# Kernel optimization log

Measured on AMD Instinct MI355X. Metric: run time of the kernel, lower is better.

## Reference

```python
import jax, jax.numpy as jnp
import numpy as np

D_MODEL = 768
N_HEADS = 12
D_K = D_MODEL // N_HEADS
WINDOW = 256
NEG_INF = -1e30


def setup_inputs() -> dict:
    key = jax.random.key(0)
    ks = jax.random.split(key, 9)
    s = 0.02
    x = jax.random.normal(ks[0], (2, 2048, D_MODEL), dtype=jnp.float32)
    Wq = jax.random.normal(ks[1], (D_MODEL, D_MODEL), dtype=jnp.float32) * s
    bq = jnp.zeros((D_MODEL,), dtype=jnp.float32)
    Wk = jax.random.normal(ks[2], (D_MODEL, D_MODEL), dtype=jnp.float32) * s
    bk = jnp.zeros((D_MODEL,), dtype=jnp.float32)
    Wv = jax.random.normal(ks[3], (D_MODEL, D_MODEL), dtype=jnp.float32) * s
    bv = jnp.zeros((D_MODEL,), dtype=jnp.float32)
    Wo = jax.random.normal(ks[4], (D_MODEL, D_MODEL), dtype=jnp.float32) * s
    bo = jnp.zeros((D_MODEL,), dtype=jnp.float32)
    return {"x": x, "Wq": Wq, "bq": bq, "Wk": Wk, "bk": bk,
            "Wv": Wv, "bv": bv, "Wo": Wo, "bo": bo}


def _window_mask(seq_len: int) -> jnp.ndarray:
    # Faithful to _apply_sliding_window_attention: scores are reshaped into
    # (nw, ws, nw, ws) windows and a causal tril is applied broadcast over BOTH
    # window indices => position (q, k) allowed iff (q % ws) >= (k % ws).
    # (seq_len here is a multiple of WINDOW, so pad/slice is a no-op.)
    if seq_len <= WINDOW:
        q = jnp.arange(seq_len)
        return q[:, None] >= jnp.arange(seq_len)[None, :]
    qmod = jnp.arange(seq_len) % WINDOW
    return qmod[:, None] >= qmod[None, :]


def reference(x, Wq, bq, Wk, bk, Wv, bv, Wo, bo):
    B, S, _ = x.shape
    # torch nn.Linear: y = x @ W.T + b
    q = (x @ Wq.T + bq).reshape(B, S, N_HEADS, D_K).transpose(0, 2, 1, 3)
    k = (x @ Wk.T + bk).reshape(B, S, N_HEADS, D_K).transpose(0, 2, 1, 3)
    v = (x @ Wv.T + bv).reshape(B, S, N_HEADS, D_K).transpose(0, 2, 1, 3)
    scores = jnp.einsum('bhqd,bhkd->bhqk', q, k) / jnp.sqrt(jnp.float32(D_K))
    mask = _window_mask(S)  # [S, S] bool
    scores = jnp.where(mask[None, None, :, :], scores, NEG_INF)
    probs = jax.nn.softmax(scores, axis=-1)  # dropout p=0 (eval)
    out = jnp.einsum('bhqk,bhkd->bhqd', probs, v)
    out = out.transpose(0, 2, 1, 3).reshape(B, S, D_MODEL)
    return out @ Wo.T + bo
```

## Files before the change

kernel.cpp:

```cpp
#include <hip/hip_runtime.h>

typedef unsigned short u16;
typedef unsigned int u32;
typedef unsigned long long u64;
typedef __attribute__((ext_vector_type(8))) short bfrag;
typedef __attribute__((ext_vector_type(4))) float f32x4;
typedef __attribute__((ext_vector_type(16))) float f32x16;
typedef __attribute__((ext_vector_type(4))) u32 u32x4;

#define QSCALE 0.18033688f

__device__ __forceinline__ u16 f2bf(float f) {
    unsigned u = __float_as_uint(f);
    u += 0x7FFFu + ((u >> 16) & 1u);
    return (u16)(u >> 16);
}

__device__ __forceinline__ u32 cvt_pk_bf16(float lo, float hi) {
    u32 r;
    asm("v_cvt_pk_bf16_f32 %0, %1, %2" : "=v"(r) : "v"(lo), "v"(hi));
    return r;
}

__device__ __forceinline__ void glds16(const void* g, void* l) {
    __builtin_amdgcn_global_load_lds((__attribute__((address_space(1))) void*)g,
                                     (__attribute__((address_space(3))) void*)l,
                                     16, 0, 0);
}

__device__ __forceinline__ f32x16 mfma32(bfrag a, bfrag b, f32x16 c) {
    return __builtin_amdgcn_mfma_f32_32x32x16_bf16(a, b, c, 0, 0, 0);
}

#define WAIT_VM4()  asm volatile("s_waitcnt vmcnt(4)" ::: "memory")
#define WAIT_VM0()  asm volatile("s_waitcnt vmcnt(0)" ::: "memory")
#define BAR()       __builtin_amdgcn_s_barrier()
#define SCHED_FENCE() __builtin_amdgcn_sched_barrier(0)

__global__ __launch_bounds__(256) void convert_all(
    const float* __restrict__ x, const float* __restrict__ wq,
    const float* __restrict__ wk, const float* __restrict__ wv,
    const float* __restrict__ wo,
    u16* __restrict__ xb, u16* __restrict__ wqb, u16* __restrict__ wkb,
    u16* __restrict__ wvb, u16* __restrict__ wob) {
    const int XV = (2 * 2048 * 768) / 4;
    const int WV = (768 * 768) / 4;
    int i = blockIdx.x * 256 + threadIdx.x;
    if (i >= XV + 4 * WV) return;
    const float4* src; u16* dst; int off;
    if (i < XV) { src = (const float4*)x; dst = xb; off = i; }
    else {
        int j = i - XV; int z = j / WV; off = j - z * WV;
        src = (const float4*)(z == 0 ? wq : z == 1 ? wk : z == 2 ? wv : wo);
        dst = (z == 0 ? wqb : z == 1 ? wkb : z == 2 ? wvb : wob);
    }
    float4 v = src[off];
    u64 pk = (u64)f2bf(v.x)
        | ((u64)f2bf(v.y) << 16)
        | ((u64)f2bf(v.z) << 32)
        | ((u64)f2bf(v.w) << 48);
    *(u64*)(dst + off * 4) = pk;
}

__device__ __forceinline__ void gemm_core(
    const u16* __restrict__ A, const u16* __restrict__ Bw, int m0,
    u16* a_lds, u16* b_lds, f32x4 acc[4][4]) {
    const int t = threadIdx.x;
    const int w = t >> 6, lane = t & 63, ln = lane & 15, lh = lane >> 4;
    const int wr = w >> 1, wc = w & 1;

    const int row0 = t >> 2;
    const int u0 = (t & 3) ^ ((row0 >> 1) & 3);
    const int row1 = row0 + 64;
    const int u1 = (t & 3) ^ ((row1 >> 1) & 3);
    const u16* ga0 = A + (m0 + row0) * 768 + u0 * 8;
    const u16* ga1 = A + (m0 + row1) * 768 + u1 * 8;
    const u16* gb0 = Bw + row0 * 768 + u0 * 8;
    const u16* gb1 = Bw + row1 * 768 + u1 * 8;
    u16* la = a_lds + w * 512;
    u16* lb = b_lds + w * 512;

    auto STAGE = [&](int k0, int bi) {
        glds16(ga0 + k0, la + bi * 4096);
        glds16(ga1 + k0, la + bi * 4096 + 2048);
        glds16(gb0 + k0, lb + bi * 4096);
        glds16(gb1 + k0, lb + bi * 4096 + 2048);
    };

    STAGE(0, 0);
    int cur = 0;
    for (int k0 = 0; k0 < 768; k0 += 32) {
        if (k0 + 32 < 768) {
            STAGE(k0 + 32, cur ^ 1);
            WAIT_VM4();
        } else {
            WAIT_VM0();
        }
        BAR();
        SCHED_FENCE();
        const u16* ab = a_lds + cur * 4096;
        const u16* bb = b_lds + cur * 4096;
        bfrag aF[4], bF[4];
#pragma unroll
        for (int i = 0; i < 4; i++) {
            int ra = wr * 64 + i * 16 + ln;
            aF[i] = *(const bfrag*)(ab + ra * 32 + ((lh ^ ((ra >> 1) & 3)) * 8));
            int rb = wc * 64 + i * 16 + ln;
            bF[i] = *(const bfrag*)(bb + rb * 32 + ((lh ^ ((rb >> 1) & 3)) * 8));
        }
#pragma unroll
        for (int i = 0; i < 4; i++)
#pragma unroll
            for (int j = 0; j < 4; j++)
                acc[i][j] = __builtin_amdgcn_mfma_f32_16x16x32_bf16(
                    aF[i], bF[j], acc[i][j], 0, 0, 0);
        SCHED_FENCE();
        BAR();
        cur ^= 1;
    }
}

__global__ __launch_bounds__(256) void gemm_qkv(
    const u16* __restrict__ xb,
    const u16* __restrict__ wqb, const u16* __restrict__ wkb, const u16* __restrict__ wvb,
    const float* __restrict__ bq, const float* __restrict__ bk, const float* __restrict__ bv,
    u16* __restrict__ q_ws, u16* __restrict__ k_ws, u16* __restrict__ vt_ws) {
    __shared__ __align__(16) u16 smem[16384];
    u16* a_lds = smem;
    u16* b_lds = smem + 8192;
    const int m0 = blockIdx.x * 128;
    const int z = blockIdx.y / 6, nb = blockIdx.y % 6;
    const u16* Bw = (z == 0 ? wqb : z == 1 ? wkb : wvb) + nb * 128 * 768;
    const float* bias = (z == 0 ? bq : z == 1 ? bk : bv);

    f32x4 acc[4][4] = {};
    gemm_core(xb, Bw, m0, a_lds, b_lds, acc);

    const int t = threadIdx.x, w = t >> 6, lane = t & 63, ln = lane & 15, lh = lane >> 4;
    const int wr = w >> 1, wc = w & 1;
    if (z == 2) {
        __syncthreads();
        char* T = (char*)smem;
#pragma unroll
        for (int j = 0; j < 4; j++) {
            int nt = wc * 64 + j * 16 + ln;
            float bb = bias[nb * 128 + nt];
#pragma unroll
            for (int i = 0; i < 4; i++) {
                int m0t = wr * 64 + i * 16 + lh * 4;
                u64 pk = (u64)f2bf(acc[i][j][0] + bb)
                    | ((u64)f2bf(acc[i][j][1] + bb) << 16)
                    | ((u64)f2bf(acc[i][j][2] + bb) << 32)
                    | ((u64)f2bf(acc[i][j][3] + bb) << 48);
                int off = nt * 256 + ((m0t * 2) ^ ((nt & 15) << 4));
                *(u64*)(T + off) = pk;
            }
        }
        __syncthreads();
        const int b = m0 >> 11, s0 = m0 & 2047;
#pragma unroll
        for (int c = 0; c < 8; c++) {
            int g = c * 256 + t;
            int nt = g >> 4, mc = (g & 15) * 8;
            int off = nt * 256 + ((mc * 2) ^ ((nt & 15) << 4));
            u32x4 v = *(const u32x4*)(T + off);
            int nl = nb * 128 + nt;
            int h = nl >> 6, d = nl & 63;
            *(u32x4*)(vt_ws + ((size_t)((b * 12 + h) * 64 + d)) * 2048 + s0 + mc) = v;
        }
    } else {
        u16* dst = (z == 0 ? q_ws : k_ws);
        const float sc = (z == 0) ? QSCALE : 1.0f;
#pragma unroll
        for (int j = 0; j < 4; j++) {
            int nl = nb * 128 + wc * 64 + j * 16 + ln;
            int h = nl >> 6, d = nl & 63;
            float bb = bias[nl];
#pragma unroll
            for (int i = 0; i < 4; i++)
#pragma unroll
                for (int r = 0; r < 4; r++) {
                    int m = m0 + wr * 64 + i * 16 + lh * 4 + r;
                    int b = m >> 11, s = m & 2047;
                    dst[((size_t)((b * 12 + h) * 2048 + s)) * 64 + d] = f2bf((acc[i][j][r] + bb) * sc);
                }
        }
    }
}

__global__ __launch_bounds__(256) void gemm_out(
    const u16* __restrict__ ob, const u16* __restrict__ wob,
    const float* __restrict__ bo, float* __restrict__ out) {
    __shared__ __align__(16) u16 a_lds[2 * 128 * 32];
    __shared__ __align__(16) u16 b_lds[2 * 128 * 32];
    const int m0 = blockIdx.x * 128, n0 = blockIdx.y * 128;
    f32x4 acc[4][4] = {};
    gemm_core(ob, wob + n0 * 768, m0, a_lds, b_lds, acc);
    const int t = threadIdx.x, w = t >> 6, lane = t & 63, ln = lane & 15, lh = lane >> 4;
    const int wr = w >> 1, wc = w & 1;
#pragma unroll
    for (int j = 0; j < 4; j++) {
        int n = n0 + wc * 64 + j * 16 + ln;
        float bb = bo[n];
#pragma unroll
        for (int i = 0; i < 4; i++)
#pragma unroll
            for (int r = 0; r < 4; r++) {
                int m = m0 + wr * 64 + i * 16 + lh * 4 + r;
                out[m * 768 + n] = acc[i][j][r] + bb;
            }
    }
}

__global__ __launch_bounds__(256) void attn7(
    const u16* __restrict__ q_ws, const u16* __restrict__ k_ws,
    const u16* __restrict__ vt_ws,
    u16* __restrict__ po_ws, float* __restrict__ l_ws) {
    __shared__ __align__(16) u16 k_lds[2][64 * 64];
    __shared__ __align__(16) u16 v_lds[2][64 * 64];

    const int t = threadIdx.x, w = t >> 6, l = t & 63, lq = l & 31, H = l >> 5;
    int id = blockIdx.x;
    int bh8 = id & 7, idq = id >> 3;
    int bhq = idq % 3, pg = idq / 3;
    int t7, rem;
    if (pg < 16)      { t7 = 7 - (pg >> 3); rem = pg & 7; }
    else if (pg < 28) { int u = pg - 16; t7 = 5 - u / 6; rem = u % 6; }
    else if (pg < 36) { int u = pg - 28; t7 = 3 - (u >> 2); rem = u & 3; }
    else              { int u = pg - 36; t7 = 1 - (u >> 1); rem = u & 1; }
    const int np = (t7 + 2) >> 1;
    const int quad = rem / np, piece = rem - quad * np;
    const int bh = bhq * 8 + bh8;
    const int ti = quad * 4 + w;
    const int tile = t7 + 8 * ti;
    const int qw0 = tile * 32;

    const u16* Qb = q_ws + (size_t)bh * 2048 * 64;
    const u16* Kb = k_ws + (size_t)bh * 2048 * 64;
    const u16* Vt = vt_ws + (size_t)bh * 64 * 2048;

    const int lqp = (lq & 19) | ((lq & 4) << 1) | ((lq & 8) >> 1);
    const int ksw = lqp & 7;
    const int vsw = lq & 7;

    bfrag qF[4];
#pragma unroll
    for (int kd = 0; kd < 4; kd++)
        qF[kd] = *(const bfrag*)(Qb + (size_t)(qw0 + lq) * 64 + kd * 16 + H * 8);

    const f32x16 Z = {};
    f32x16 O0 = Z, O1 = Z;
    float lsum = 0.f;

    const int skey = t >> 3;
    const int su = (t & 7) ^ (skey & 7);

    auto STAGE = [&](int k0, int bi) {
        glds16(Kb + (size_t)(k0 + skey) * 64 + su * 8,        k_lds[bi] + w * 512);
        glds16(Kb + (size_t)(k0 + skey + 32) * 64 + su * 8,   k_lds[bi] + 2048 + w * 512);
        glds16(Vt + (size_t)skey * 2048 + k0 + su * 8,        v_lds[bi] + w * 512);
        glds16(Vt + (size_t)(skey + 32) * 2048 + k0 + su * 8, v_lds[bi] + 2048 + w * 512);
    };

    int gp0 = piece * 8;
    int win = gp0 / np, pb = gp0 - win * np;
    STAGE(win * 256 + pb * 64, 0);

    for (int j = 0; j < 8; ++j) {
        int winn = win, pbn = pb + 1;
        if (pbn == np) { pbn = 0; winn = win + 1; }
        if (j < 7) {
            STAGE(winn * 256 + pbn * 64, (j + 1) & 1);
            WAIT_VM4();
        } else {
            WAIT_VM0();
        }
        BAR();
        SCHED_FENCE();

        const int cb = 2 * pb;
        const bool c1 = (cb + 1) <= t7, d0 = (cb == t7), d1 = (cb + 1 == t7);
        const u16* kl = k_lds[j & 1];
        const u16* vl = v_lds[j & 1];

        f32x16 s0, s1;
        {
            bfrag kf = *(const bfrag*)(kl + lqp * 64 + ((H) ^ ksw) * 8);
            s0 = mfma32(kf, qF[0], Z);
#pragma unroll
            for (int kd = 1; kd < 4; kd++) {
                bfrag k2 = *(const bfrag*)(kl + lqp * 64 + ((kd * 2 + H) ^ ksw) * 8);
                s0 = mfma32(k2, qF[kd], s0);
            }
        }
        if (c1) {
            bfrag kf = *(const bfrag*)(kl + (32 + lqp) * 64 + ((H) ^ ksw) * 8);
            s1 = mfma32(kf, qF[0], Z);
#pragma unroll
            for (int kd = 1; kd < 4; kd++) {
                bfrag k2 = *(const bfrag*)(kl + (32 + lqp) * 64 + ((kd * 2 + H) ^ ksw) * 8);
                s1 = mfma32(k2, qF[kd], s1);
            }
        }

        float ps = 0.f;
        u32 pkA[8], pkB[8];
        if (d0) {
#pragma unroll
            for (int r2 = 0; r2 < 16; r2++) {
                int ka = (r2 & 3) + 4 * ((r2 >> 2) & 1) + 16 * (r2 >> 3) + 8 * H;
                if (ka > lq) s0[r2] = -1e30f;
            }
        }
#pragma unroll
        for (int i = 0; i < 8; i++) {
            float a = exp2f(s0[2 * i]), b2 = exp2f(s0[2 * i + 1]);
            ps += a + b2; pkA[i] = cvt_pk_bf16(a, b2);
        }
        if (c1) {
            if (d1) {
#pragma unroll
                for (int r2 = 0; r2 < 16; r2++) {
                    int ka = (r2 & 3) + 4 * ((r2 >> 2) & 1) + 16 * (r2 >> 3) + 8 * H;
                    if (ka > lq) s1[r2] = -1e30f;
                }
            }
#pragma unroll
            for (int i = 0; i < 8; i++) {
                float a = exp2f(s1[2 * i]), b2 = exp2f(s1[2 * i + 1]);
                ps += a + b2; pkB[i] = cvt_pk_bf16(a, b2);
            }
        }
        lsum += ps;

        {
            u32x4 a0 = {pkA[0], pkA[1], pkA[2], pkA[3]};
            u32x4 a1 = {pkA[4], pkA[5], pkA[6], pkA[7]};
            bfrag A0 = __builtin_bit_cast(bfrag, a0);
            bfrag A1 = __builtin_bit_cast(bfrag, a1);
            bfrag v00 = *(const bfrag*)(vl + lq * 64 + ((H) ^ vsw) * 8);
            bfrag v01 = *(const bfrag*)(vl + (32 + lq) * 64 + ((H) ^ vsw) * 8);
            bfrag v10 = *(const bfrag*)(vl + lq * 64 + ((2 + H) ^ vsw) * 8);
            bfrag v11 = *(const bfrag*)(vl + (32 + lq) * 64 + ((2 + H) ^ vsw) * 8);
            O0 = mfma32(A0, v00, O0);
            O1 = mfma32(A0, v01, O1);
            O0 = mfma32(A1, v10, O0);
            O1 = mfma32(A1, v11, O1);
        }
        if (c1) {
            u32x4 a0 = {pkB[0], pkB[1], pkB[2], pkB[3]};
            u32x4 a1 = {pkB[4], pkB[5], pkB[6], pkB[7]};
            bfrag A0 = __builtin_bit_cast(bfrag, a0);
            bfrag A1 = __builtin_bit_cast(bfrag, a1);
            bfrag v00 = *(const bfrag*)(vl + lq * 64 + ((4 + H) ^ vsw) * 8);
            bfrag v01 = *(const bfrag*)(vl + (32 + lq) * 64 + ((4 + H) ^ vsw) * 8);
            bfrag v10 = *(const bfrag*)(vl + lq * 64 + ((6 + H) ^ vsw) * 8);
            bfrag v11 = *(const bfrag*)(vl + (32 + lq) * 64 + ((6 + H) ^ vsw) * 8);
            O0 = mfma32(A0, v00, O0);
            O1 = mfma32(A0, v01, O1);
            O0 = mfma32(A1, v10, O0);
            O1 = mfma32(A1, v11, O1);
        }
        SCHED_FENCE();
        BAR();
        win = winn; pb = pbn;
    }

    const int cum8[8] = {0, 8, 16, 32, 48, 72, 96, 128};
    size_t pidx = (size_t)bh * 160 + cum8[t7] + ti * np + piece;
    u16* po = po_ws + pidx * 2048;
#pragma unroll
    for (int r2 = 0; r2 < 16; r2++) {
        int row = (r2 & 3) + 8 * (r2 >> 2) + 4 * H;
        po[row * 64 + lq] = f2bf(O0[r2]);
        po[row * 64 + 32 + lq] = f2bf(O1[r2]);
    }
    float lsT = lsum + __shfl_xor(lsum, 32);
    if (l < 32) l_ws[pidx * 32 + lq] = lsT;
}

__global__ __launch_bounds__(256) void combine_o(
    const u16* __restrict__ po_ws, const float* __restrict__ l_ws,
    u16* __restrict__ o_ws) {
    int id = blockIdx.x;
    int bh8 = id & 7, idq = id >> 3;
    int bhq = idq % 3, r = idq / 3;
    int bh = bhq * 8 + bh8;
    int t7 = r >> 3, ti = r & 7;
    int tile = t7 + 8 * ti;
    int np = (t7 + 2) >> 1;
    const int cum8[8] = {0, 8, 16, 32, 48, 72, 96, 128};
    size_t base = (size_t)bh * 160 + cum8[t7] + ti * np;
    int t = threadIdx.x;
    int q = t >> 3, d8 = (t & 7) * 8;
    float acc[8] = {0.f, 0.f, 0.f, 0.f, 0.f, 0.f, 0.f, 0.f};
    float lt = 0.f;
    for (int i = 0; i < np; i++) {
        lt += l_ws[(base + i) * 32 + q];
        bfrag v = *(const bfrag*)(po_ws + (base + i) * 2048 + q * 64 + d8);
#pragma unroll
        for (int e = 0; e < 8; e++)
            acc[e] += __uint_as_float(((u32)(u16)v[e]) << 16);
    }
    float inv = 1.f / lt;
    u32x4 pkv;
#pragma unroll
    for (int e = 0; e < 4; e++)
        pkv[e] = cvt_pk_bf16(acc[2 * e] * inv, acc[2 * e + 1] * inv);
    int b = bh / 12, h = bh % 12;
    size_t dst = ((size_t)(b * 2048 + tile * 32 + q)) * 768 + h * 64 + d8;
    *(u32x4*)(o_ws + dst) = pkv;
}

extern "C" void kernel_launch(void* const* d_in, const int* in_sizes, int n_in,
                              void* d_out, int out_size, void* d_ws, size_t ws_size,
                              hipStream_t stream) {
    const float* x  = (const float*)d_in[0];
    const float* Wq = (const float*)d_in[1];
    const float* bq = (const float*)d_in[2];
    const float* Wk = (const float*)d_in[3];
    const float* bk = (const float*)d_in[4];
    const float* Wv = (const float*)d_in[5];
    const float* bv = (const float*)d_in[6];
    const float* Wo = (const float*)d_in[7];
    const float* bo = (const float*)d_in[8];
    float* out = (float*)d_out;

    char* p = (char*)d_ws;
    u16*   q_ws  = (u16*)(p + 0);
    u16*   k_ws  = (u16*)(p + 6291456);
    u16*   vt_ws = (u16*)(p + 12582912);
    u16*   po_ws = (u16*)(p + 18874368);
    u16*   xb    = (u16*)(p + 18874368);
    u16*   wqb   = (u16*)(p + 25165824);
    u16*   wkb   = (u16*)(p + 26345472);
    u16*   wvb   = (u16*)(p + 27525120);
    float* l_ws  = (float*)(p + 34603008);
    u16*   wob   = (u16*)(p + 35094528);
    u16*   o_ws  = (u16*)(p + 0);

    convert_all<<<5376, 256, 0, stream>>>(x, Wq, Wk, Wv, Wo, xb, wqb, wkb, wvb, wob);
    gemm_qkv<<<dim3(32, 18), 256, 0, stream>>>(xb, wqb, wkb, wvb, bq, bk, bv, q_ws, k_ws, vt_ws);
    attn7<<<dim3(960), 256, 0, stream>>>(q_ws, k_ws, vt_ws, po_ws, l_ws);
    combine_o<<<dim3(1536), 256, 0, stream>>>(po_ws, l_ws, o_ws);
    gemm_out<<<dim3(32, 6), 256, 0, stream>>>(o_ws, wob, bo, out);
}
```

Before: 95.45 us.

## Finalize single-piece attention tiles in-kernel, shrink output GEMM tile, add MFMA priority

Attention tiles that have only one KV piece (t7 0 and 1) now normalize by the row sum and write straight to the output-activation buffer. combine_o then launches only for the multi-piece tiles, which saves partial-output round trips and combine work. The output projection switches to a 64x128 tile with 16x16x32 MFMA, doubling the grid to 384 blocks for better occupancy across CUs. s_setprio is also placed around the MFMA sections in the attention loop. o_ws is moved to its own workspace region, so it no longer aliases q_ws.

```diff
diff --git a/kernel.cpp b/kernel.cpp
--- a/kernel.cpp
+++ b/kernel.cpp
@@ -33,9 +33,11 @@
 }
 
 #define WAIT_VM4()  asm volatile("s_waitcnt vmcnt(4)" ::: "memory")
+#define WAIT_VM3()  asm volatile("s_waitcnt vmcnt(3)" ::: "memory")
 #define WAIT_VM0()  asm volatile("s_waitcnt vmcnt(0)" ::: "memory")
 #define BAR()       __builtin_amdgcn_s_barrier()
 #define SCHED_FENCE() __builtin_amdgcn_sched_barrier(0)
+#define PRIO(n)     __builtin_amdgcn_s_setprio(n)
 
 __global__ __launch_bounds__(256) void convert_all(
     const float* __restrict__ x, const float* __restrict__ wq,
@@ -188,33 +190,84 @@
     }
 }
 
-__global__ __launch_bounds__(256) void gemm_out(
+__global__ __launch_bounds__(256) void gemm_out64(
     const u16* __restrict__ ob, const u16* __restrict__ wob,
     const float* __restrict__ bo, float* __restrict__ out) {
-    __shared__ __align__(16) u16 a_lds[2 * 128 * 32];
+    __shared__ __align__(16) u16 a_lds[2 * 64 * 32];
     __shared__ __align__(16) u16 b_lds[2 * 128 * 32];
-    const int m0 = blockIdx.x * 128, n0 = blockIdx.y * 128;
-    f32x4 acc[4][4] = {};
-    gemm_core(ob, wob + n0 * 768, m0, a_lds, b_lds, acc);
-    const int t = threadIdx.x, w = t >> 6, lane = t & 63, ln = lane & 15, lh = lane >> 4;
+    const int m0 = blockIdx.x * 64, n0 = blockIdx.y * 128;
+    const int t = threadIdx.x;
+    const int w = t >> 6, lane = t & 63, ln = lane & 15, lh = lane >> 4;
     const int wr = w >> 1, wc = w & 1;
+
+    const int rowA = t >> 2;
+    const int uA = (t & 3) ^ ((rowA >> 1) & 3);
+    const int rowB1 = rowA + 64;
+    const int uB1 = (t & 3) ^ ((rowB1 >> 1) & 3);
+    const u16* ga  = ob + (m0 + rowA) * 768 + uA * 8;
+    const u16* gb0 = wob + (n0 + rowA) * 768 + uA * 8;
+    const u16* gb1 = wob + (n0 + rowB1) * 768 + uB1 * 8;
+    u16* la = a_lds + w * 512;
+    u16* lb = b_lds + w * 512;
+
+    auto STAGE = [&](int k0, int bi) {
+        glds16(ga + k0, la + bi * 2048);
+        glds16(gb0 + k0, lb + bi * 4096);
+        glds16(gb1 + k0, lb + bi * 4096 + 2048);
+    };
+
+    f32x4 acc[2][4] = {};
+    STAGE(0, 0);
+    int cur = 0;
+    for (int k0 = 0; k0 < 768; k0 += 32) {
+        if (k0 + 32 < 768) {
+            STAGE(k0 + 32, cur ^ 1);
+            WAIT_VM3();
+        } else {
+            WAIT_VM0();
+        }
+        BAR();
+        SCHED_FENCE();
+        const u16* ab = a_lds + cur * 2048;
+        const u16* bb = b_lds + cur * 4096;
+        bfrag aF[2], bF[4];
+#pragma unroll
+        for (int i = 0; i < 2; i++) {
+            int ra = wr * 32 + i * 16 + ln;
+            aF[i] = *(const bfrag*)(ab + ra * 32 + ((lh ^ ((ra >> 1) & 3)) * 8));
+        }
+#pragma unroll
+        for (int j = 0; j < 4; j++) {
+            int rb = wc * 64 + j * 16 + ln;
+            bF[j] = *(const bfrag*)(bb + rb * 32 + ((lh ^ ((rb >> 1) & 3)) * 8));
+        }
+#pragma unroll
+        for (int i = 0; i < 2; i++)
+#pragma unroll
+            for (int j = 0; j < 4; j++)
+                acc[i][j] = __builtin_amdgcn_mfma_f32_16x16x32_bf16(
+                    aF[i], bF[j], acc[i][j], 0, 0, 0);
+        SCHED_FENCE();
+        BAR();
+        cur ^= 1;
+    }
 #pragma unroll
     for (int j = 0; j < 4; j++) {
         int n = n0 + wc * 64 + j * 16 + ln;
         float bb = bo[n];
 #pragma unroll
-        for (int i = 0; i < 4; i++)
+        for (int i = 0; i < 2; i++)
 #pragma unroll
             for (int r = 0; r < 4; r++) {
-                int m = m0 + wr * 64 + i * 16 + lh * 4 + r;
+                int m = m0 + wr * 32 + i * 16 + lh * 4 + r;
                 out[m * 768 + n] = acc[i][j][r] + bb;
             }
     }
 }
 
-__global__ __launch_bounds__(256) void attn7(
+__global__ __launch_bounds__(256) void attn8(
     const u16* __restrict__ q_ws, const u16* __restrict__ k_ws,
-    const u16* __restrict__ vt_ws,
+    const u16* __restrict__ vt_ws, u16* __restrict__ o_ws,
     u16* __restrict__ po_ws, float* __restrict__ l_ws) {
     __shared__ __align__(16) u16 k_lds[2][64 * 64];
     __shared__ __align__(16) u16 v_lds[2][64 * 64];
@@ -283,6 +336,7 @@
         const u16* kl = k_lds[j & 1];
         const u16* vl = v_lds[j & 1];
 
+        PRIO(1);
         f32x16 s0, s1;
         {
             bfrag kf = *(const bfrag*)(kl + lqp * 64 + ((H) ^ ksw) * 8);
@@ -302,6 +356,7 @@
                 s1 = mfma32(k2, qF[kd], s1);
             }
         }
+        PRIO(0);
 
         float ps = 0.f;
         u32 pkA[8], pkB[8];
@@ -333,6 +388,7 @@
         }
         lsum += ps;
 
+        PRIO(1);
         {
             u32x4 a0 = {pkA[0], pkA[1], pkA[2], pkA[3]};
             u32x4 a1 = {pkA[4], pkA[5], pkA[6], pkA[7]};
@@ -361,22 +417,36 @@
             O0 = mfma32(A1, v10, O0);
             O1 = mfma32(A1, v11, O1);
         }
+        PRIO(0);
         SCHED_FENCE();
         BAR();
         win = winn; pb = pbn;
     }
 
-    const int cum8[8] = {0, 8, 16, 32, 48, 72, 96, 128};
-    size_t pidx = (size_t)bh * 160 + cum8[t7] + ti * np + piece;
-    u16* po = po_ws + pidx * 2048;
-#pragma unroll
-    for (int r2 = 0; r2 < 16; r2++) {
-        int row = (r2 & 3) + 8 * (r2 >> 2) + 4 * H;
-        po[row * 64 + lq] = f2bf(O0[r2]);
-        po[row * 64 + 32 + lq] = f2bf(O1[r2]);
-    }
     float lsT = lsum + __shfl_xor(lsum, 32);
-    if (l < 32) l_ws[pidx * 32 + lq] = lsT;
+    if (np == 1) {
+        float linv = 1.f / lsT;
+        const int b = bh / 12, h = bh % 12;
+#pragma unroll
+        for (int r2 = 0; r2 < 16; r2++) {
+            int row = (r2 & 3) + 8 * (r2 >> 2) + 4 * H;
+            float fr = __shfl(linv, row);
+            size_t base = ((size_t)(b * 2048 + qw0 + row)) * 768 + h * 64;
+            o_ws[base + lq] = f2bf(O0[r2] * fr);
+            o_ws[base + 32 + lq] = f2bf(O1[r2] * fr);
+        }
+    } else {
+        const int cum8[8] = {0, 8, 16, 32, 48, 72, 96, 128};
+        size_t pidx = (size_t)bh * 160 + cum8[t7] + ti * np + piece;
+        u16* po = po_ws + pidx * 2048;
+#pragma unroll
+        for (int r2 = 0; r2 < 16; r2++) {
+            int row = (r2 & 3) + 8 * (r2 >> 2) + 4 * H;
+            po[row * 64 + lq] = f2bf(O0[r2]);
+            po[row * 64 + 32 + lq] = f2bf(O1[r2]);
+        }
+        if (l < 32) l_ws[pidx * 32 + lq] = lsT;
+    }
 }
 
 __global__ __launch_bounds__(256) void combine_o(
@@ -386,7 +456,7 @@
     int bh8 = id & 7, idq = id >> 3;
     int bhq = idq % 3, r = idq / 3;
     int bh = bhq * 8 + bh8;
-    int t7 = r >> 3, ti = r & 7;
+    int t7 = 2 + (r >> 3), ti = r & 7;
     int tile = t7 + 8 * ti;
     int np = (t7 + 2) >> 1;
     const int cum8[8] = {0, 8, 16, 32, 48, 72, 96, 128};
@@ -437,11 +507,11 @@
     u16*   wvb   = (u16*)(p + 27525120);
     float* l_ws  = (float*)(p + 34603008);
     u16*   wob   = (u16*)(p + 35094528);
-    u16*   o_ws  = (u16*)(p + 0);
+    u16*   o_ws  = (u16*)(p + 36274176);
 
     convert_all<<<5376, 256, 0, stream>>>(x, Wq, Wk, Wv, Wo, xb, wqb, wkb, wvb, wob);
     gemm_qkv<<<dim3(32, 18), 256, 0, stream>>>(xb, wqb, wkb, wvb, bq, bk, bv, q_ws, k_ws, vt_ws);
-    attn7<<<dim3(960), 256, 0, stream>>>(q_ws, k_ws, vt_ws, po_ws, l_ws);
-    combine_o<<<dim3(1536), 256, 0, stream>>>(po_ws, l_ws, o_ws);
-    gemm_out<<<dim3(32, 6), 256, 0, stream>>>(o_ws, wob, bo, out);
-}
+    attn8<<<dim3(960), 256, 0, stream>>>(q_ws, k_ws, vt_ws, o_ws, po_ws, l_ws);
+    combine_o<<<dim3(1152), 256, 0, stream>>>(po_ws, l_ws, o_ws);
+    gemm_out64<<<dim3(64, 6), 256, 0, stream>>>(o_ws, wob, bo, out);
+}
```

Result: faster. 90.95 us (-4.7%).
